# Kernel optimization log

Hardware: AMD Instinct MI355X
Metric: run time of the kernel (lower is better)

## Reference

```python
import jax, jax.numpy as jnp
import numpy as np

N, D, M, L, DEPTH, WIDTH, MPTS = 2048, 64, 2048, 16, 3, 128, 64
WIN = 2 * L + 1  # 33


def setup_inputs() -> dict:
    key = jax.random.key(0)
    ks = jax.random.split(key, 6)
    # xavier-normal-ish scales to keep sigmoids in a reasonable range
    s0 = float(np.sqrt(2.0 / (D + WIDTH)))
    s1 = float(np.sqrt(2.0 / (2 * WIDTH)))
    s2 = float(np.sqrt(2.0 / (WIDTH + WIN)))
    return {
        "u": jax.random.normal(ks[0], (MPTS, D), dtype=jnp.float32),
        "weight0": jax.random.normal(ks[1], (WIN, WIDTH, D), dtype=jnp.float32) * s0,
        "bias0": jnp.zeros((WIN, WIDTH, 1), dtype=jnp.float32),
        "weight": jax.random.normal(ks[2], (DEPTH - 1, WIN, WIDTH, WIDTH), dtype=jnp.float32) * s1,
        "bias": jnp.zeros((DEPTH - 1, WIN, WIDTH, 1), dtype=jnp.float32),
        "weight_final": jax.random.normal(ks[3], (M, WIN, WIDTH), dtype=jnp.float32) * s2,
        "bias_final": jnp.zeros((M, WIN, 1), dtype=jnp.float32),
        "xi": jax.random.normal(ks[4], (M, N + 2 * L), dtype=jnp.float32) * 0.1,
    }


def reference(u, weight0, bias0, weight, bias, weight_final, bias_final, xi):
    sig = jax.nn.sigmoid
    # first_step: shared per-frequency MLP stack
    u1 = sig(jnp.einsum('jkl,ml->jkm', weight0, u) + bias0)
    for i in range(weight.shape[0]):  # depth-1 hidden layers (small fixed count)
        u1 = sig(jnp.einsum('jkl,jlm->jkm', weight[i], u1) + bias[i])
    G = sig(jnp.einsum('ijk,jkm->ijm', weight_final, u1) + bias_final)
    # sliding-window weighted sum over spectral coeffs, vectorized as a 1D
    # cross-correlation: out[n, p] = sum_{m,j} xi[m, n+j] * G[m, j, p]
    kernel = jnp.transpose(G, (2, 0, 1))
    out = jax.lax.conv_general_dilated(
        xi[None],  # [1, M, N+2L]
        kernel,
        window_strides=(1,),
        padding='VALID',
        dimension_numbers=('NCH', 'OIH', 'NCH'),
    )  # [1, MPTS, N]
    return out[0].T  # [N, MPTS] == torch.cat over iter_prod
```

## Files before the change

### kernel.cpp

```cpp
#include <hip/hip_runtime.h>

#define WIN 33
#define WIDTH 128
#define MPTS 64
#define NN 2048
#define MM 2048
#define DD 64
#define NQ 2080

typedef __bf16 bf16x8 __attribute__((ext_vector_type(8)));
typedef float f32x4 __attribute__((ext_vector_type(4)));

__device__ __forceinline__ unsigned short f2bf(float x) {
  union { float f; unsigned int u; } v; v.f = x;
  unsigned int r = v.u + 0x7FFFu + ((v.u >> 16) & 1u);
  return (unsigned short)(r >> 16);
}
__device__ __forceinline__ float sigf(float x) { return 1.0f / (1.0f + __expf(-x)); }

__device__ __forceinline__ void gll16(const unsigned short* g, unsigned short* l) {
  __builtin_amdgcn_global_load_lds(
      (const __attribute__((address_space(1))) unsigned int*)g,
      (__attribute__((address_space(3))) unsigned int*)l, 16, 0, 0);
}

__global__ __launch_bounds__(256) void k_prep(const float* __restrict__ xi,
                                              unsigned short* __restrict__ xiT,
                                              const float* __restrict__ u,
                                              const float* __restrict__ w0,
                                              const float* __restrict__ b0,
                                              const float* __restrict__ w,
                                              const float* __restrict__ bias,
                                              unsigned short* __restrict__ u1bf,
                                              float* __restrict__ out) {
  extern __shared__ char smem[];
  int bid = blockIdx.x;
  int tid = threadIdx.x;

  if (bid < 33) {
    constexpr int WS = 72;
    constexpr int AS = 136;
    float* biass = (float*)smem;
    unsigned short* ws   = (unsigned short*)(smem + 512);
    unsigned short* actA = (unsigned short*)(smem + 18944);
    unsigned short* actB = (unsigned short*)(smem + 36352);
    int j = bid;
    int wv = tid >> 6, lane = tid & 63, l15 = lane & 15, l4 = lane >> 4;

#pragma unroll
    for (int c = tid; c < 1024; c += 256) {
      int p = c >> 4, d4 = (c & 15) << 2;
      float4 v = *(const float4*)&u[(size_t)p * DD + d4];
      ushort4 h; h.x = f2bf(v.x); h.y = f2bf(v.y); h.z = f2bf(v.z); h.w = f2bf(v.w);
      *(ushort4*)&actA[p * AS + d4] = h;
    }
#pragma unroll
    for (int c = tid; c < 2048; c += 256) {
      int k = c >> 4, d4 = (c & 15) << 2;
      float4 v = *(const float4*)&w0[((size_t)j * 128 + k) * DD + d4];
      ushort4 h; h.x = f2bf(v.x); h.y = f2bf(v.y); h.z = f2bf(v.z); h.w = f2bf(v.w);
      *(ushort4*)&ws[k * WS + d4] = h;
    }
    if (tid < 128) biass[tid] = b0[j * 128 + tid];
    __syncthreads();

    {
      f32x4 acc[2][4] = {};
#pragma unroll
      for (int t = 0; t < 2; ++t) {
        int col = (t << 5) + (l4 << 3);
        bf16x8 a[2], b[4];
#pragma unroll
        for (int s = 0; s < 2; ++s)
          a[s] = *(const bf16x8*)&ws[(wv * 32 + s * 16 + l15) * WS + col];
#pragma unroll
        for (int q = 0; q < 4; ++q)
          b[q] = *(const bf16x8*)&actA[(q * 16 + l15) * AS + col];
#pragma unroll
        for (int s = 0; s < 2; ++s)
#pragma unroll
          for (int q = 0; q < 4; ++q)
            acc[s][q] = __builtin_amdgcn_mfma_f32_16x16x32_bf16(a[s], b[q], acc[s][q], 0, 0, 0);
      }
#pragma unroll
      for (int s = 0; s < 2; ++s)
#pragma unroll
        for (int q = 0; q < 4; ++q) {
          int p = q * 16 + l15;
#pragma unroll
          for (int r = 0; r < 4; ++r) {
            int k = wv * 32 + s * 16 + (l4 << 2) + r;
            actB[p * AS + k] = f2bf(sigf(acc[s][q][r] + biass[k]));
          }
        }
    }

    unsigned short* ain = actB;
    unsigned short* aout = actA;
#pragma unroll
    for (int i = 0; i < 2; ++i) {
      f32x4 acc[2][4] = {};
      const float* wbase = w + ((size_t)i * WIN + j) * 128 * 128;
#pragma unroll
      for (int h = 0; h < 2; ++h) {
        __syncthreads();
#pragma unroll
        for (int c = tid; c < 2048; c += 256) {
          int k = c >> 4, d4 = (c & 15) << 2;
          float4 v = *(const float4*)&wbase[(size_t)k * 128 + h * 64 + d4];
          ushort4 hh; hh.x = f2bf(v.x); hh.y = f2bf(v.y); hh.z = f2bf(v.z); hh.w = f2bf(v.w);
          *(ushort4*)&ws[k * WS + d4] = hh;
        }
        if (h == 0 && tid < 128) biass[tid] = bias[((size_t)i * WIN + j) * 128 + tid];
        __syncthreads();
#pragma unroll
        for (int t = 0; t < 2; ++t) {
          int col = (t << 5) + (l4 << 3);
          bf16x8 a[2], b[4];
#pragma unroll
          for (int s = 0; s < 2; ++s)
            a[s] = *(const bf16x8*)&ws[(wv * 32 + s * 16 + l15) * WS + col];
#pragma unroll
          for (int q = 0; q < 4; ++q)
            b[q] = *(const bf16x8*)&ain[(q * 16 + l15) * AS + h * 64 + col];
#pragma unroll
          for (int s = 0; s < 2; ++s)
#pragma unroll
            for (int q = 0; q < 4; ++q)
              acc[s][q] = __builtin_amdgcn_mfma_f32_16x16x32_bf16(a[s], b[q], acc[s][q], 0, 0, 0);
        }
      }
#pragma unroll
      for (int s = 0; s < 2; ++s)
#pragma unroll
        for (int q = 0; q < 4; ++q) {
          int p = q * 16 + l15;
#pragma unroll
          for (int r = 0; r < 4; ++r) {
            int k = wv * 32 + s * 16 + (l4 << 2) + r;
            aout[p * AS + k] = f2bf(sigf(acc[s][q][r] + biass[k]));
          }
        }
      unsigned short* t2 = ain; ain = aout; aout = t2;
    }
    __syncthreads();
#pragma unroll
    for (int c = tid; c < 1024; c += 256) {
      int p = c >> 4, k8 = (c & 15) << 3;
      uint4 v = *(const uint4*)&ain[p * AS + k8];
      *(uint4*)&u1bf[((size_t)j * MPTS + p) * WIDTH + k8] = v;
    }
  } else {
    float* ts = (float*)smem;
    int t = bid - 33;
    if (t < 512 && tid < 64) {
      float4 z = {0.f, 0.f, 0.f, 0.f};
      *(float4*)&out[((size_t)t << 8) + (tid << 2)] = z;
    }
    int qt = t % 65, mt = t / 65;
    int qb = qt * 32;
    int mb = mt * 64;
#pragma unroll
    for (int c = tid; c < 512; c += 256) {
      int row = c >> 3, c8 = c & 7;
      float4 v = *(const float4*)&xi[(size_t)(mb + row) * NQ + qb + (c8 << 2)];
      ts[row * 37 + (c8 << 2) + 0] = v.x;
      ts[row * 37 + (c8 << 2) + 1] = v.y;
      ts[row * 37 + (c8 << 2) + 2] = v.z;
      ts[row * 37 + (c8 << 2) + 3] = v.w;
    }
    __syncthreads();
#pragma unroll
    for (int c = tid; c < 512; c += 256) {
      int r = c >> 4, mq = c & 15;
      ushort4 h;
      h.x = f2bf(ts[(mq * 4 + 0) * 37 + r]);
      h.y = f2bf(ts[(mq * 4 + 1) * 37 + r]);
      h.z = f2bf(ts[(mq * 4 + 2) * 37 + r]);
      h.w = f2bf(ts[(mq * 4 + 3) * 37 + r]);
      *(ushort4*)&xiT[((size_t)mt * NQ + (qb + r)) * 64 + (mq << 2)] = h;
    }
  }
}

__global__ __launch_bounds__(256) void k_final(const float* __restrict__ wf,
                                               const float* __restrict__ bfin,
                                               const unsigned short* __restrict__ u1bf,
                                               unsigned short* __restrict__ Gt2) {
  constexpr int KP = 136;
  __shared__ unsigned short As[64 * KP];
  __shared__ unsigned short Bs[64 * KP];
  __shared__ float bfs[64];
  int bid = blockIdx.x;
  int j = bid >> 5;
  int m0 = (bid & 31) << 6;
#pragma unroll
  for (int c = threadIdx.x; c < 64 * 32; c += 256) {
    int row = c >> 5, f4 = c & 31;
    float4 v = *(const float4*)(wf + ((size_t)(m0 + row) * WIN + j) * WIDTH + (f4 << 2));
    ushort4 h;
    h.x = f2bf(v.x); h.y = f2bf(v.y); h.z = f2bf(v.z); h.w = f2bf(v.w);
    *(ushort4*)(&As[row * KP + (f4 << 2)]) = h;
  }
#pragma unroll
  for (int c = threadIdx.x; c < 64 * 16; c += 256) {
    int p = c >> 4, ch = c & 15;
    uint4 v = *(const uint4*)(u1bf + (size_t)(j * MPTS + p) * WIDTH + (ch << 3));
    *(uint4*)(&Bs[p * KP + (ch << 3)]) = v;
  }
  if (threadIdx.x < 64) bfs[threadIdx.x] = bfin[(size_t)(m0 + threadIdx.x) * WIN + j];
  __syncthreads();
  int wv = threadIdx.x >> 6, lane = threadIdx.x & 63;
  int l15 = lane & 15, l4 = lane >> 4;
  f32x4 acc[4] = {};
#pragma unroll
  for (int t = 0; t < 4; ++t) {
    int col = (t << 5) + (l4 << 3);
    bf16x8 a = *(const bf16x8*)(&As[(wv * 16 + l15) * KP + col]);
#pragma unroll
    for (int q = 0; q < 4; ++q) {
      bf16x8 bb = *(const bf16x8*)(&Bs[(q * 16 + l15) * KP + col]);
      acc[q] = __builtin_amdgcn_mfma_f32_16x16x32_bf16(a, bb, acc[q], 0, 0, 0);
    }
  }
  size_t region = (size_t)((bid & 31) << 1) + (wv >> 1);
  int g = ((wv & 1) << 1) + (l4 >> 1);
  int m8 = (l4 & 1) << 2;
  int mb = wv * 16 + (l4 << 2);
#pragma unroll
  for (int q = 0; q < 4; ++q) {
    int p = q * 16 + l15;
    float z0 = acc[q][0] + bfs[mb + 0];
    float z1 = acc[q][1] + bfs[mb + 1];
    float z2 = acc[q][2] + bfs[mb + 2];
    float z3 = acc[q][3] + bfs[mb + 3];
    ushort4 st;
    st.x = f2bf(sigf(z0)); st.y = f2bf(sigf(z1));
    st.z = f2bf(sigf(z2)); st.w = f2bf(sigf(z3));
    *(ushort4*)(&Gt2[region * 67584 + ((size_t)(j * 4 + g) * 64 + p) * 8 + m8]) = st;
  }
}

__global__ __launch_bounds__(256) void k_conv(const unsigned short* __restrict__ xiT,
                                              const unsigned short* __restrict__ Gt2,
                                              float* __restrict__ out) {
  extern __shared__ unsigned short lds[];
  unsigned short* As = lds;
  int bid = blockIdx.x;
  int mp = bid & 31;
  int n0 = (bid >> 5) << 7;
  int tid = threadIdx.x;
  int wv = tid >> 6, lane = tid & 63, l15 = lane & 15, l4 = lane >> 4;

  const unsigned short* Abase = xiT + (size_t)mp * (NQ * 64) + (size_t)n0 * 64;
#pragma unroll
  for (int k = 0; k < 5; ++k) {
    int instr = wv * 5 + k;
    int s = (instr << 6) + lane;
    int row = s >> 3;
    int c = (s & 7) ^ (row & 7);
    gll16(Abase + (size_t)row * 64 + (c << 3), As + (instr << 9));
  }

  constexpr int JBT[10]  = {0, 7, 14, 21, 28, 0, 7, 14, 21, 28};
  constexpr int CNTT[10] = {7, 7, 7, 7, 5, 7, 7, 7, 7, 5};
  constexpr int HFT[10]  = {0, 0, 0, 0, 0, 1, 1, 1, 1, 1};

  const unsigned short* Rb0 = Gt2 + (size_t)(mp << 1) * 67584;
  const unsigned short* Rb1 = Gt2 + (size_t)((mp << 1) + 1) * 67584;

  {
    const unsigned short* Bb = Rb0;
#pragma unroll
    for (int k = 0; k < 7; ++k) {
      int instr = wv * 7 + k;
      gll16(Bb + (((instr << 6) + lane) << 3), lds + 10240 + (instr << 9));
    }
  }

  f32x4 acc[2][4] = {};
#pragma unroll
  for (int t = 0; t < 10; ++t) {
    __syncthreads();
    if (t < 9) {
      const int jbn = JBT[t + 1], cntn = CNTT[t + 1];
      const unsigned short* Bb =
          (HFT[t + 1] ? Rb1 : Rb0) + ((size_t)jbn << 11);
      unsigned short* Bst = lds + 10240 + ((t + 1) & 1) * 14336;
#pragma unroll
      for (int k = 0; k < cntn; ++k) {
        int instr = wv * cntn + k;
        gll16(Bb + (((instr << 6) + lane) << 3), Bst + (instr << 9));
      }
    }
    {
      const int jb = JBT[t], cnt = CNTT[t], h4 = HFT[t] << 2;
      const unsigned short* Bs = lds + 10240 + (t & 1) * 14336;
      bf16x8 a[2], b[4];
#pragma unroll
      for (int s = 0; s < 2; ++s) {
        int row = wv * 32 + s * 16 + l15 + jb;
        a[s] = *(const bf16x8*)&As[row * 64 + (((h4 | l4) ^ (row & 7)) << 3)];
      }
#pragma unroll
      for (int q = 0; q < 4; ++q) {
        int slot = (l4 << 6) + (q << 4) + l15;
        b[q] = *(const bf16x8*)&Bs[slot << 3];
      }
#pragma unroll
      for (int jj = 0; jj < cnt; ++jj) {
        bf16x8 an[2], bn[4];
        if (jj < cnt - 1) {
#pragma unroll
          for (int s = 0; s < 2; ++s) {
            int row = wv * 32 + s * 16 + l15 + jb + jj + 1;
            an[s] = *(const bf16x8*)&As[row * 64 + (((h4 | l4) ^ (row & 7)) << 3)];
          }
#pragma unroll
          for (int q = 0; q < 4; ++q) {
            int slot = ((((jj + 1) << 2) + l4) << 6) + (q << 4) + l15;
            bn[q] = *(const bf16x8*)&Bs[slot << 3];
          }
        }
#pragma unroll
        for (int s = 0; s < 2; ++s)
#pragma unroll
          for (int q = 0; q < 4; ++q)
            acc[s][q] = __builtin_amdgcn_mfma_f32_16x16x32_bf16(a[s], b[q], acc[s][q], 0, 0, 0);
#pragma unroll
        for (int s = 0; s < 2; ++s) a[s] = an[s];
#pragma unroll
        for (int q = 0; q < 4; ++q) b[q] = bn[q];
      }
    }
  }
#pragma unroll
  for (int s = 0; s < 2; ++s)
#pragma unroll
    for (int q = 0; q < 4; ++q) {
      int nr = n0 + wv * 32 + s * 16 + (l4 << 2);
      int p = q * 16 + l15;
#pragma unroll
      for (int i = 0; i < 4; ++i)
        atomicAdd(&out[(size_t)(nr + i) * MPTS + p], acc[s][q][i]);
    }
}

extern "C" void kernel_launch(void* const* d_in, const int* in_sizes, int n_in,
                              void* d_out, int out_size, void* d_ws, size_t ws_size,
                              hipStream_t stream) {
  const float* u    = (const float*)d_in[0];
  const float* w0   = (const float*)d_in[1];
  const float* b0   = (const float*)d_in[2];
  const float* w    = (const float*)d_in[3];
  const float* bias = (const float*)d_in[4];
  const float* wf   = (const float*)d_in[5];
  const float* bfin = (const float*)d_in[6];
  const float* xi   = (const float*)d_in[7];
  float* out = (float*)d_out;
  char* ws = (char*)d_ws;
  unsigned short* xiT  = (unsigned short*)(ws);
  unsigned short* Gt2  = (unsigned short*)(ws + 8519680);
  unsigned short* u1bf = (unsigned short*)(ws + 17170432);

  hipFuncSetAttribute(reinterpret_cast<const void*>(&k_prep),
                      hipFuncAttributeMaxDynamicSharedMemorySize, 53760);
  hipFuncSetAttribute(reinterpret_cast<const void*>(&k_conv),
                      hipFuncAttributeMaxDynamicSharedMemorySize, 77824);

  k_prep<<<2113, 256, 53760, stream>>>(xi, xiT, u, w0, b0, w, bias, u1bf, out);
  k_final<<<33 * 32, 256, 0, stream>>>(wf, bfin, u1bf, Gt2);
  k_conv<<<512, 256, 77824, stream>>>(xiT, Gt2, out);
}
```

Before: 153.3 us.

## Split conv window taps across waves and reduce partial tiles through LDS

The conv kernel now splits the window taps of each stage across the four waves, so each wave computes the full 128x64 output tile for its own taps, instead of each wave owning 32 rows across all taps. Each wave reads one B fragment per tap for 32 MFMAs, which raises reuse of B reads and gives more independent MFMA chains per wave. The partial tiles are summed serially through LDS, and then one atomicAdd per output element is issued, cutting global atomics fourfold. In exchange the accumulator grows to 128 floats per thread, which raises register pressure; launch bounds of 2 blocks per SIMD are requested. Waves 1-3 idle on the 5-tap stages (only 8 of 10 per stage cover work per wave in pairs), adding load imbalance and serialized reduction barriers.

Measured after the change: 183.3 us. 19.6% more time.

```diff
diff --git a/kernel.cpp b/kernel.cpp
--- a/kernel.cpp
+++ b/kernel.cpp
@@ -241,9 +241,9 @@
   }
 }
 
-__global__ __launch_bounds__(256) void k_conv(const unsigned short* __restrict__ xiT,
-                                              const unsigned short* __restrict__ Gt2,
-                                              float* __restrict__ out) {
+__global__ __launch_bounds__(256, 2) void k_conv(const unsigned short* __restrict__ xiT,
+                                                 const unsigned short* __restrict__ Gt2,
+                                                 float* __restrict__ out) {
   extern __shared__ unsigned short lds[];
   unsigned short* As = lds;
   int bid = blockIdx.x;
@@ -278,7 +278,7 @@
     }
   }
 
-  f32x4 acc[2][4] = {};
+  f32x4 acc[8][4] = {};
 #pragma unroll
   for (int t = 0; t < 10; ++t) {
     __syncthreads();
@@ -296,54 +296,51 @@
     {
       const int jb = JBT[t], cnt = CNTT[t], h4 = HFT[t] << 2;
       const unsigned short* Bs = lds + 10240 + (t & 1) * 14336;
-      bf16x8 a[2], b[4];
-#pragma unroll
-      for (int s = 0; s < 2; ++s) {
-        int row = wv * 32 + s * 16 + l15 + jb;
-        a[s] = *(const bf16x8*)&As[row * 64 + (((h4 | l4) ^ (row & 7)) << 3)];
+#pragma unroll
+      for (int r = 0; r < 2; ++r) {
+        int jj = wv + (r << 2);
+        if (jj < cnt) {
+          bf16x8 a[8], b[4];
+#pragma unroll
+          for (int g = 0; g < 8; ++g) {
+            int row = (g << 4) + l15 + jb + jj;
+            a[g] = *(const bf16x8*)&As[row * 64 + (((h4 | l4) ^ (row & 7)) << 3)];
+          }
+#pragma unroll
+          for (int q = 0; q < 4; ++q) {
+            int slot = (((jj << 2) + l4) << 6) + (q << 4) + l15;
+            b[q] = *(const bf16x8*)&Bs[slot << 3];
+          }
+#pragma unroll
+          for (int g = 0; g < 8; ++g)
+#pragma unroll
+            for (int q = 0; q < 4; ++q)
+              acc[g][q] = __builtin_amdgcn_mfma_f32_16x16x32_bf16(a[g], b[q], acc[g][q], 0, 0, 0);
+        }
       }
-#pragma unroll
-      for (int q = 0; q < 4; ++q) {
-        int slot = (l4 << 6) + (q << 4) + l15;
-        b[q] = *(const bf16x8*)&Bs[slot << 3];
-      }
-#pragma unroll
-      for (int jj = 0; jj < cnt; ++jj) {
-        bf16x8 an[2], bn[4];
-        if (jj < cnt - 1) {
-#pragma unroll
-          for (int s = 0; s < 2; ++s) {
-            int row = wv * 32 + s * 16 + l15 + jb + jj + 1;
-            an[s] = *(const bf16x8*)&As[row * 64 + (((h4 | l4) ^ (row & 7)) << 3)];
-          }
-#pragma unroll
-          for (int q = 0; q < 4; ++q) {
-            int slot = ((((jj + 1) << 2) + l4) << 6) + (q << 4) + l15;
-            bn[q] = *(const bf16x8*)&Bs[slot << 3];
-          }
-        }
-#pragma unroll
-        for (int s = 0; s < 2; ++s)
-#pragma unroll
-          for (int q = 0; q < 4; ++q)
-            acc[s][q] = __builtin_amdgcn_mfma_f32_16x16x32_bf16(a[s], b[q], acc[s][q], 0, 0, 0);
-#pragma unroll
-        for (int s = 0; s < 2; ++s) a[s] = an[s];
-#pragma unroll
-        for (int q = 0; q < 4; ++q) b[q] = bn[q];
-      }
-    }
-  }
-#pragma unroll
-  for (int s = 0; s < 2; ++s)
-#pragma unroll
-    for (int q = 0; q < 4; ++q) {
-      int nr = n0 + wv * 32 + s * 16 + (l4 << 2);
-      int p = q * 16 + l15;
-#pragma unroll
-      for (int i = 0; i < 4; ++i)
-        atomicAdd(&out[(size_t)(nr + i) * MPTS + p], acc[s][q][i]);
-    }
+    }
+  }
+
+  float* red = (float*)lds;
+#pragma unroll 1
+  for (int w = 0; w < 4; ++w) {
+    __syncthreads();
+    if (wv == w) {
+#pragma unroll
+      for (int g = 0; g < 8; ++g)
+#pragma unroll
+        for (int q = 0; q < 4; ++q)
+#pragma unroll
+          for (int i = 0; i < 4; ++i) {
+            int idx = (((g << 4) + (l4 << 2) + i) << 6) + (q << 4) + l15;
+            if (w == 0) red[idx] = acc[g][q][i];
+            else        red[idx] += acc[g][q][i];
+          }
+    }
+  }
+  __syncthreads();
+  for (int c = tid; c < 8192; c += 256)
+    atomicAdd(&out[((size_t)(n0 + (c >> 6)) << 6) + (c & 63)], red[c]);
 }
 
 extern "C" void kernel_launch(void* const* d_in, const int* in_sizes, int n_in,
```

## Prefetch next MLP weight half into registers while MFMA runs

Applied to the files above, without the earlier changes.

The per-frequency MLP stage is restructured into a software pipeline. The global loads for the next 64-column weight half are issued into registers before the MFMA work on the current half, then converted to bf16 and written to LDS after a barrier. The goal is to hide global-load latency behind matrix math, where before each load and compute step ran in strict sequence. In exchange, the 8 float4 staging registers per thread raise register pressure, and only the 33 MLP blocks benefit.

Result: faster. 146.3 us (-4.6%).

```diff
diff --git a/kernel.cpp b/kernel.cpp
--- a/kernel.cpp
+++ b/kernel.cpp
@@ -47,25 +47,25 @@
     int j = bid;
     int wv = tid >> 6, lane = tid & 63, l15 = lane & 15, l4 = lane >> 4;
 
-#pragma unroll
-    for (int c = tid; c < 1024; c += 256) {
-      int p = c >> 4, d4 = (c & 15) << 2;
-      float4 v = *(const float4*)&u[(size_t)p * DD + d4];
-      ushort4 h; h.x = f2bf(v.x); h.y = f2bf(v.y); h.z = f2bf(v.z); h.w = f2bf(v.w);
-      *(ushort4*)&actA[p * AS + d4] = h;
-    }
-#pragma unroll
-    for (int c = tid; c < 2048; c += 256) {
-      int k = c >> 4, d4 = (c & 15) << 2;
-      float4 v = *(const float4*)&w0[((size_t)j * 128 + k) * DD + d4];
-      ushort4 h; h.x = f2bf(v.x); h.y = f2bf(v.y); h.z = f2bf(v.z); h.w = f2bf(v.w);
-      *(ushort4*)&ws[k * WS + d4] = h;
-    }
-    if (tid < 128) biass[tid] = b0[j * 128 + tid];
-    __syncthreads();
-
-    {
-      f32x4 acc[2][4] = {};
+    float4 wreg[8];
+
+    auto wload = [&](const float* src) {
+#pragma unroll
+      for (int r = 0; r < 8; ++r) {
+        int c = tid + (r << 8);
+        wreg[r] = *(const float4*)&src[(size_t)(c >> 4) * 128 + ((c & 15) << 2)];
+      }
+    };
+    auto wstore = [&]() {
+#pragma unroll
+      for (int r = 0; r < 8; ++r) {
+        int c = tid + (r << 8);
+        float4 v = wreg[r];
+        ushort4 h; h.x = f2bf(v.x); h.y = f2bf(v.y); h.z = f2bf(v.z); h.w = f2bf(v.w);
+        *(ushort4*)&ws[(c >> 4) * WS + ((c & 15) << 2)] = h;
+      }
+    };
+    auto mma_half = [&](const unsigned short* bsrc, int hofs, f32x4 (&acc)[2][4]) {
 #pragma unroll
       for (int t = 0; t < 2; ++t) {
         int col = (t << 5) + (l4 << 3);
@@ -75,13 +75,15 @@
           a[s] = *(const bf16x8*)&ws[(wv * 32 + s * 16 + l15) * WS + col];
 #pragma unroll
         for (int q = 0; q < 4; ++q)
-          b[q] = *(const bf16x8*)&actA[(q * 16 + l15) * AS + col];
+          b[q] = *(const bf16x8*)&bsrc[(q * 16 + l15) * AS + hofs + col];
 #pragma unroll
         for (int s = 0; s < 2; ++s)
 #pragma unroll
           for (int q = 0; q < 4; ++q)
             acc[s][q] = __builtin_amdgcn_mfma_f32_16x16x32_bf16(a[s], b[q], acc[s][q], 0, 0, 0);
       }
+    };
+    auto sigstore = [&](f32x4 (&acc)[2][4], unsigned short* dst) {
 #pragma unroll
       for (int s = 0; s < 2; ++s)
 #pragma unroll
@@ -90,64 +92,78 @@
 #pragma unroll
           for (int r = 0; r < 4; ++r) {
             int k = wv * 32 + s * 16 + (l4 << 2) + r;
-            actB[p * AS + k] = f2bf(sigf(acc[s][q][r] + biass[k]));
+            dst[p * AS + k] = f2bf(sigf(acc[s][q][r] + biass[k]));
           }
         }
-    }
-
-    unsigned short* ain = actB;
-    unsigned short* aout = actA;
-#pragma unroll
-    for (int i = 0; i < 2; ++i) {
-      f32x4 acc[2][4] = {};
-      const float* wbase = w + ((size_t)i * WIN + j) * 128 * 128;
-#pragma unroll
-      for (int h = 0; h < 2; ++h) {
-        __syncthreads();
-#pragma unroll
-        for (int c = tid; c < 2048; c += 256) {
-          int k = c >> 4, d4 = (c & 15) << 2;
-          float4 v = *(const float4*)&wbase[(size_t)k * 128 + h * 64 + d4];
-          ushort4 hh; hh.x = f2bf(v.x); hh.y = f2bf(v.y); hh.z = f2bf(v.z); hh.w = f2bf(v.w);
-          *(ushort4*)&ws[k * WS + d4] = hh;
-        }
-        if (h == 0 && tid < 128) biass[tid] = bias[((size_t)i * WIN + j) * 128 + tid];
-        __syncthreads();
-#pragma unroll
-        for (int t = 0; t < 2; ++t) {
-          int col = (t << 5) + (l4 << 3);
-          bf16x8 a[2], b[4];
-#pragma unroll
-          for (int s = 0; s < 2; ++s)
-            a[s] = *(const bf16x8*)&ws[(wv * 32 + s * 16 + l15) * WS + col];
-#pragma unroll
-          for (int q = 0; q < 4; ++q)
-            b[q] = *(const bf16x8*)&ain[(q * 16 + l15) * AS + h * 64 + col];
-#pragma unroll
-          for (int s = 0; s < 2; ++s)
-#pragma unroll
-            for (int q = 0; q < 4; ++q)
-              acc[s][q] = __builtin_amdgcn_mfma_f32_16x16x32_bf16(a[s], b[q], acc[s][q], 0, 0, 0);
-        }
-      }
-#pragma unroll
-      for (int s = 0; s < 2; ++s)
-#pragma unroll
-        for (int q = 0; q < 4; ++q) {
-          int p = q * 16 + l15;
-#pragma unroll
-          for (int r = 0; r < 4; ++r) {
-            int k = wv * 32 + s * 16 + (l4 << 2) + r;
-            aout[p * AS + k] = f2bf(sigf(acc[s][q][r] + biass[k]));
-          }
-        }
-      unsigned short* t2 = ain; ain = aout; aout = t2;
-    }
+    };
+
+    const float* wb0 = w + ((size_t)0 * WIN + j) * 16384;
+    const float* wb1 = w + ((size_t)1 * WIN + j) * 16384;
+
+    {
+      float4 ureg[4];
+#pragma unroll
+      for (int r = 0; r < 4; ++r) {
+        int c = tid + (r << 8);
+        ureg[r] = *(const float4*)&u[(size_t)(c >> 4) * DD + ((c & 15) << 2)];
+      }
+#pragma unroll
+      for (int r = 0; r < 8; ++r) {
+        int c = tid + (r << 8);
+        wreg[r] = *(const float4*)&w0[((size_t)j * 128 + (c >> 4)) * DD + ((c & 15) << 2)];
+      }
+      if (tid < 128) biass[tid] = b0[j * 128 + tid];
+#pragma unroll
+      for (int r = 0; r < 4; ++r) {
+        int c = tid + (r << 8);
+        float4 v = ureg[r];
+        ushort4 h; h.x = f2bf(v.x); h.y = f2bf(v.y); h.z = f2bf(v.z); h.w = f2bf(v.w);
+        *(ushort4*)&actA[(c >> 4) * AS + ((c & 15) << 2)] = h;
+      }
+#pragma unroll
+      for (int r = 0; r < 8; ++r) {
+        int c = tid + (r << 8);
+        float4 v = wreg[r];
+        ushort4 h; h.x = f2bf(v.x); h.y = f2bf(v.y); h.z = f2bf(v.z); h.w = f2bf(v.w);
+        *(ushort4*)&ws[(c >> 4) * WS + ((c & 15) << 2)] = h;
+      }
+    }
+    __syncthreads();
+
+    f32x4 acc0[2][4] = {};
+    wload(wb0 + 0);
+    mma_half(actA, 0, acc0);
+    sigstore(acc0, actB);
+    __syncthreads();
+    wstore();
+    if (tid < 128) biass[tid] = bias[(size_t)j * 128 + tid];
+    __syncthreads();
+    f32x4 acc1[2][4] = {};
+    wload(wb0 + 64);
+    mma_half(actB, 0, acc1);
+    __syncthreads();
+    wstore();
+    __syncthreads();
+    wload(wb1 + 0);
+    mma_half(actB, 64, acc1);
+    sigstore(acc1, actA);
+    __syncthreads();
+    wstore();
+    if (tid < 128) biass[tid] = bias[(size_t)(WIN + j) * 128 + tid];
+    __syncthreads();
+    f32x4 acc2[2][4] = {};
+    wload(wb1 + 64);
+    mma_half(actA, 0, acc2);
+    __syncthreads();
+    wstore();
+    __syncthreads();
+    mma_half(actA, 64, acc2);
+    sigstore(acc2, actB);
     __syncthreads();
 #pragma unroll
     for (int c = tid; c < 1024; c += 256) {
       int p = c >> 4, k8 = (c & 15) << 3;
-      uint4 v = *(const uint4*)&ain[p * AS + k8];
+      uint4 v = *(const uint4*)&actB[p * AS + k8];
       *(uint4*)&u1bf[((size_t)j * MPTS + p) * WIDTH + k8] = v;
     }
   } else {
```

## Load MLP weights straight into registers and prefetch all layers up front

Applied to the files above, without the earlier changes.

In the 33 MLP blocks of k_prep, weight tiles are no longer staged through shared memory. Each lane loads its MFMA A-operand fragments directly from global memory into registers and converts them to bf16 in registers. All three layers' weights and biases are issued at the start (layer 2 after the first barrier), so load latency overlaps the earlier layers and several __syncthreads are removed. Sigmoid outputs are written as ushort4, and the last layer stores straight to global, which drops the LDS copy-out and shrinks dynamic shared memory. The cost is much higher register pressure (about 160 VGPRs held for weights), which risks spills or lower occupancy in the other k_prep blocks.

After: 146.6 us. -4.3%, faster.

```diff
diff --git a/kernel.cpp b/kernel.cpp
--- a/kernel.cpp
+++ b/kernel.cpp
@@ -22,6 +22,13 @@
   __builtin_amdgcn_global_load_lds(
       (const __attribute__((address_space(1))) unsigned int*)g,
       (__attribute__((address_space(3))) unsigned int*)l, 16, 0, 0);
+}
+
+__device__ __forceinline__ bf16x8 cvt8(const float4& a, const float4& b) {
+  union { bf16x8 v; unsigned short s[8]; } u;
+  u.s[0] = f2bf(a.x); u.s[1] = f2bf(a.y); u.s[2] = f2bf(a.z); u.s[3] = f2bf(a.w);
+  u.s[4] = f2bf(b.x); u.s[5] = f2bf(b.y); u.s[6] = f2bf(b.z); u.s[7] = f2bf(b.w);
+  return u.v;
 }
 
 __global__ __launch_bounds__(256) void k_prep(const float* __restrict__ xi,
@@ -38,41 +45,77 @@
   int tid = threadIdx.x;
 
   if (bid < 33) {
-    constexpr int WS = 72;
     constexpr int AS = 136;
     float* biass = (float*)smem;
-    unsigned short* ws   = (unsigned short*)(smem + 512);
-    unsigned short* actA = (unsigned short*)(smem + 18944);
-    unsigned short* actB = (unsigned short*)(smem + 36352);
+    unsigned short* actA = (unsigned short*)(smem + 1536);
+    unsigned short* actB = (unsigned short*)(smem + 18944);
     int j = bid;
     int wv = tid >> 6, lane = tid & 63, l15 = lane & 15, l4 = lane >> 4;
-
-#pragma unroll
-    for (int c = tid; c < 1024; c += 256) {
-      int p = c >> 4, d4 = (c & 15) << 2;
-      float4 v = *(const float4*)&u[(size_t)p * DD + d4];
-      ushort4 h; h.x = f2bf(v.x); h.y = f2bf(v.y); h.z = f2bf(v.z); h.w = f2bf(v.w);
-      *(ushort4*)&actA[p * AS + d4] = h;
-    }
-#pragma unroll
-    for (int c = tid; c < 2048; c += 256) {
-      int k = c >> 4, d4 = (c & 15) << 2;
-      float4 v = *(const float4*)&w0[((size_t)j * 128 + k) * DD + d4];
-      ushort4 h; h.x = f2bf(v.x); h.y = f2bf(v.y); h.z = f2bf(v.z); h.w = f2bf(v.w);
-      *(ushort4*)&ws[k * WS + d4] = h;
-    }
-    if (tid < 128) biass[tid] = b0[j * 128 + tid];
+    int colb = l4 << 3;
+
+    const float* wb0 = w + (size_t)j * 16384;
+    const float* wb1 = w + (size_t)(WIN + j) * 16384;
+
+    float4 wr0[8], wr1[16], wr2[16];
+
+    {
+      float4 ureg[4];
+#pragma unroll
+      for (int r = 0; r < 4; ++r) {
+        int c = tid + (r << 8);
+        ureg[r] = *(const float4*)&u[(size_t)(c >> 4) * DD + ((c & 15) << 2)];
+      }
+#pragma unroll
+      for (int s = 0; s < 2; ++s)
+#pragma unroll
+        for (int t = 0; t < 2; ++t) {
+          int row = wv * 32 + s * 16 + l15, col = (t << 5) + colb;
+          const float* p = &w0[((size_t)j * 128 + row) * 64 + col];
+          wr0[(s * 2 + t) * 2 + 0] = *(const float4*)p;
+          wr0[(s * 2 + t) * 2 + 1] = *(const float4*)(p + 4);
+        }
+#pragma unroll
+      for (int s = 0; s < 2; ++s)
+#pragma unroll
+        for (int t = 0; t < 4; ++t) {
+          int row = wv * 32 + s * 16 + l15, col = (t << 5) + colb;
+          const float* p = &wb0[(size_t)row * 128 + col];
+          wr1[(s * 4 + t) * 2 + 0] = *(const float4*)p;
+          wr1[(s * 4 + t) * 2 + 1] = *(const float4*)(p + 4);
+        }
+      if (tid < 128) {
+        biass[tid]       = b0[j * 128 + tid];
+        biass[128 + tid] = bias[(size_t)j * 128 + tid];
+        biass[256 + tid] = bias[(size_t)(WIN + j) * 128 + tid];
+      }
+#pragma unroll
+      for (int r = 0; r < 4; ++r) {
+        int c = tid + (r << 8);
+        float4 v = ureg[r];
+        ushort4 h; h.x = f2bf(v.x); h.y = f2bf(v.y); h.z = f2bf(v.z); h.w = f2bf(v.w);
+        *(ushort4*)&actA[(c >> 4) * AS + ((c & 15) << 2)] = h;
+      }
+    }
     __syncthreads();
 
+#pragma unroll
+    for (int s = 0; s < 2; ++s)
+#pragma unroll
+      for (int t = 0; t < 4; ++t) {
+        int row = wv * 32 + s * 16 + l15, col = (t << 5) + colb;
+        const float* p = &wb1[(size_t)row * 128 + col];
+        wr2[(s * 4 + t) * 2 + 0] = *(const float4*)p;
+        wr2[(s * 4 + t) * 2 + 1] = *(const float4*)(p + 4);
+      }
     {
       f32x4 acc[2][4] = {};
 #pragma unroll
       for (int t = 0; t < 2; ++t) {
-        int col = (t << 5) + (l4 << 3);
+        int col = (t << 5) + colb;
         bf16x8 a[2], b[4];
 #pragma unroll
         for (int s = 0; s < 2; ++s)
-          a[s] = *(const bf16x8*)&ws[(wv * 32 + s * 16 + l15) * WS + col];
+          a[s] = cvt8(wr0[(s * 2 + t) * 2], wr0[(s * 2 + t) * 2 + 1]);
 #pragma unroll
         for (int q = 0; q < 4; ++q)
           b[q] = *(const bf16x8*)&actA[(q * 16 + l15) * AS + col];
@@ -87,68 +130,82 @@
 #pragma unroll
         for (int q = 0; q < 4; ++q) {
           int p = q * 16 + l15;
-#pragma unroll
-          for (int r = 0; r < 4; ++r) {
-            int k = wv * 32 + s * 16 + (l4 << 2) + r;
-            actB[p * AS + k] = f2bf(sigf(acc[s][q][r] + biass[k]));
-          }
-        }
-    }
-
-    unsigned short* ain = actB;
-    unsigned short* aout = actA;
-#pragma unroll
-    for (int i = 0; i < 2; ++i) {
+          int k0 = wv * 32 + s * 16 + (l4 << 2);
+          ushort4 st;
+          st.x = f2bf(sigf(acc[s][q][0] + biass[k0 + 0]));
+          st.y = f2bf(sigf(acc[s][q][1] + biass[k0 + 1]));
+          st.z = f2bf(sigf(acc[s][q][2] + biass[k0 + 2]));
+          st.w = f2bf(sigf(acc[s][q][3] + biass[k0 + 3]));
+          *(ushort4*)&actB[p * AS + k0] = st;
+        }
+    }
+    __syncthreads();
+
+    {
       f32x4 acc[2][4] = {};
-      const float* wbase = w + ((size_t)i * WIN + j) * 128 * 128;
-#pragma unroll
-      for (int h = 0; h < 2; ++h) {
-        __syncthreads();
-#pragma unroll
-        for (int c = tid; c < 2048; c += 256) {
-          int k = c >> 4, d4 = (c & 15) << 2;
-          float4 v = *(const float4*)&wbase[(size_t)k * 128 + h * 64 + d4];
-          ushort4 hh; hh.x = f2bf(v.x); hh.y = f2bf(v.y); hh.z = f2bf(v.z); hh.w = f2bf(v.w);
-          *(ushort4*)&ws[k * WS + d4] = hh;
-        }
-        if (h == 0 && tid < 128) biass[tid] = bias[((size_t)i * WIN + j) * 128 + tid];
-        __syncthreads();
-#pragma unroll
-        for (int t = 0; t < 2; ++t) {
-          int col = (t << 5) + (l4 << 3);
-          bf16x8 a[2], b[4];
-#pragma unroll
-          for (int s = 0; s < 2; ++s)
-            a[s] = *(const bf16x8*)&ws[(wv * 32 + s * 16 + l15) * WS + col];
+#pragma unroll
+      for (int t = 0; t < 4; ++t) {
+        int col = (t << 5) + colb;
+        bf16x8 a[2], b[4];
+#pragma unroll
+        for (int s = 0; s < 2; ++s)
+          a[s] = cvt8(wr1[(s * 4 + t) * 2], wr1[(s * 4 + t) * 2 + 1]);
+#pragma unroll
+        for (int q = 0; q < 4; ++q)
+          b[q] = *(const bf16x8*)&actB[(q * 16 + l15) * AS + col];
+#pragma unroll
+        for (int s = 0; s < 2; ++s)
 #pragma unroll
           for (int q = 0; q < 4; ++q)
-            b[q] = *(const bf16x8*)&ain[(q * 16 + l15) * AS + h * 64 + col];
-#pragma unroll
-          for (int s = 0; s < 2; ++s)
-#pragma unroll
-            for (int q = 0; q < 4; ++q)
-              acc[s][q] = __builtin_amdgcn_mfma_f32_16x16x32_bf16(a[s], b[q], acc[s][q], 0, 0, 0);
-        }
+            acc[s][q] = __builtin_amdgcn_mfma_f32_16x16x32_bf16(a[s], b[q], acc[s][q], 0, 0, 0);
       }
 #pragma unroll
       for (int s = 0; s < 2; ++s)
 #pragma unroll
         for (int q = 0; q < 4; ++q) {
           int p = q * 16 + l15;
-#pragma unroll
-          for (int r = 0; r < 4; ++r) {
-            int k = wv * 32 + s * 16 + (l4 << 2) + r;
-            aout[p * AS + k] = f2bf(sigf(acc[s][q][r] + biass[k]));
-          }
-        }
-      unsigned short* t2 = ain; ain = aout; aout = t2;
+          int k0 = wv * 32 + s * 16 + (l4 << 2);
+          ushort4 st;
+          st.x = f2bf(sigf(acc[s][q][0] + biass[128 + k0 + 0]));
+          st.y = f2bf(sigf(acc[s][q][1] + biass[128 + k0 + 1]));
+          st.z = f2bf(sigf(acc[s][q][2] + biass[128 + k0 + 2]));
+          st.w = f2bf(sigf(acc[s][q][3] + biass[128 + k0 + 3]));
+          *(ushort4*)&actA[p * AS + k0] = st;
+        }
     }
     __syncthreads();
-#pragma unroll
-    for (int c = tid; c < 1024; c += 256) {
-      int p = c >> 4, k8 = (c & 15) << 3;
-      uint4 v = *(const uint4*)&ain[p * AS + k8];
-      *(uint4*)&u1bf[((size_t)j * MPTS + p) * WIDTH + k8] = v;
+
+    {
+      f32x4 acc[2][4] = {};
+#pragma unroll
+      for (int t = 0; t < 4; ++t) {
+        int col = (t << 5) + colb;
+        bf16x8 a[2], b[4];
+#pragma unroll
+        for (int s = 0; s < 2; ++s)
+          a[s] = cvt8(wr2[(s * 4 + t) * 2], wr2[(s * 4 + t) * 2 + 1]);
+#pragma unroll
+        for (int q = 0; q < 4; ++q)
+          b[q] = *(const bf16x8*)&actA[(q * 16 + l15) * AS + col];
+#pragma unroll
+        for (int s = 0; s < 2; ++s)
+#pragma unroll
+          for (int q = 0; q < 4; ++q)
+            acc[s][q] = __builtin_amdgcn_mfma_f32_16x16x32_bf16(a[s], b[q], acc[s][q], 0, 0, 0);
+      }
+#pragma unroll
+      for (int s = 0; s < 2; ++s)
+#pragma unroll
+        for (int q = 0; q < 4; ++q) {
+          int p = q * 16 + l15;
+          int k0 = wv * 32 + s * 16 + (l4 << 2);
+          ushort4 st;
+          st.x = f2bf(sigf(acc[s][q][0] + biass[256 + k0 + 0]));
+          st.y = f2bf(sigf(acc[s][q][1] + biass[256 + k0 + 1]));
+          st.z = f2bf(sigf(acc[s][q][2] + biass[256 + k0 + 2]));
+          st.w = f2bf(sigf(acc[s][q][3] + biass[256 + k0 + 3]));
+          *(ushort4*)&u1bf[((size_t)j * MPTS + p) * WIDTH + k0] = st;
+        }
     }
   } else {
     float* ts = (float*)smem;
@@ -364,11 +421,11 @@
   unsigned short* u1bf = (unsigned short*)(ws + 17170432);
 
   hipFuncSetAttribute(reinterpret_cast<const void*>(&k_prep),
-                      hipFuncAttributeMaxDynamicSharedMemorySize, 53760);
+                      hipFuncAttributeMaxDynamicSharedMemorySize, 36352);
   hipFuncSetAttribute(reinterpret_cast<const void*>(&k_conv),
                       hipFuncAttributeMaxDynamicSharedMemorySize, 77824);
 
-  k_prep<<<2113, 256, 53760, stream>>>(xi, xiT, u, w0, b0, w, bias, u1bf, out);
+  k_prep<<<2113, 256, 36352, stream>>>(xi, xiT, u, w0, b0, w, bias, u1bf, out);
   k_final<<<33 * 32, 256, 0, stream>>>(wf, bfin, u1bf, Gt2);
   k_conv<<<512, 256, 77824, stream>>>(xiT, Gt2, out);
 }
```
